# Kernel optimization log

Measured on AMD Instinct MI355X. Metric: run time of the kernel, lower is better.

Reference implementation:

```python
import jax, jax.numpy as jnp
import numpy as np

N, C_TOTAL, C, H, W = 8, 448, 100, 56, 56


def setup_inputs() -> dict:
    key = jax.random.key(0)
    k1, k2, k3, k4 = jax.random.split(key, 4)
    fmaps = jax.random.normal(k1, (N, C_TOTAL, H, W), dtype=jnp.float32)
    select_index = jax.random.randint(k2, (C,), 0, C_TOTAL)
    mean = jax.random.normal(k3, (C, H, W), dtype=jnp.float32)
    # Per-pixel inverse covariance must be PSD so the quadratic form is >= 0
    A = jax.random.normal(k4, (C, C, H, W), dtype=jnp.float32)
    cov = jnp.einsum('cehw,dehw->cdhw', A, A) / jnp.float32(C)  # (C,C,H,W), PSD per pixel
    return {
        'fmaps': fmaps,
        'select_index': select_index,
        'mean': mean,
        'cov': cov,
        'min_score': jnp.float32(0.0),
        'max_score': jnp.float32(50.0),
    }


def reference(fmaps, select_index, mean, cov, min_score, max_score):
    # x_ = fmaps[:, select_index, ...] - mean  -> (N, C, H, W)
    x = fmaps[:, select_index, :, :] - mean[None]
    # left = sum_c x[n,c,h,w] * cov[c,d,h,w]  (per-pixel matvec), avoids (N,C,C,H,W) intermediate
    left = jnp.einsum('nchw,cdhw->ndhw', x, cov)
    # per-pixel Mahalanobis distance
    s_map = jnp.sqrt(jnp.sum(x * left, axis=1))  # (N, H, W)
    # bilinear upsample x4 (torch Upsample align_corners=False == half-pixel linear resize)
    score_map = jax.image.resize(s_map, (s_map.shape[0], 4 * H, 4 * W), method='linear')
    scores = (score_map - min_score) / (max_score - min_score)
    return jnp.squeeze(scores)
```

## Files before the change

### kernel.cpp

```cpp
#include <hip/hip_runtime.h>
#include <math.h>

#define NN 8
#define C_TOTAL 448
#define CC 100
#define HH 56
#define WW 56
#define HW (HH*WW)
#define OH 224
#define OW 224
#define CT 10
#define DT 4
#define NCHUNK (CC/CT)
#define NTILE (HW/64)

__global__ __launch_bounds__(512) void qform_kernel(
    const float* __restrict__ fmaps, const int* __restrict__ sel,
    const float* __restrict__ mean, const float* __restrict__ cov,
    float* __restrict__ qpart)
{
    const int tile  = blockIdx.x % NTILE;
    const int chunk = blockIdx.x / NTILE;
    const int n     = threadIdx.x >> 6;
    const int pix   = tile * 64 + (threadIdx.x & 63);
    const int c0    = chunk * CT;

    __shared__ int s_sel[CC];
    if (threadIdx.x < CC) s_sel[threadIdx.x] = sel[threadIdx.x];
    __syncthreads();

    const float* fm_n = fmaps + (size_t)n * C_TOTAL * HW;

    float xc[CT];
#pragma unroll
    for (int i = 0; i < CT; ++i) {
        const int c = c0 + i;
        xc[i] = fm_n[(size_t)s_sel[c] * HW + pix] - mean[(size_t)c * HW + pix];
    }

    float acc = 0.0f;
    for (int d0 = 0; d0 < CC; d0 += DT) {
        float xd[DT];
#pragma unroll
        for (int j = 0; j < DT; ++j) {
            const int d = d0 + j;
            xd[j] = fm_n[(size_t)s_sel[d] * HW + pix] - mean[(size_t)d * HW + pix];
        }
#pragma unroll
        for (int i = 0; i < CT; ++i) {
            const float* cp = cov + ((size_t)(c0 + i) * CC + d0) * HW + pix;
#pragma unroll
            for (int j = 0; j < DT; ++j) {
                acc = fmaf(xc[i] * xd[j], cp[(size_t)j * HW], acc);
            }
        }
    }
    qpart[((size_t)chunk * NN + n) * HW + pix] = acc;
}

__global__ __launch_bounds__(256) void reduce_kernel(
    const float* __restrict__ qpart, float* __restrict__ smap)
{
    const int idx = blockIdx.x * 256 + threadIdx.x;
    if (idx >= NN * HW) return;
    float s = 0.0f;
#pragma unroll
    for (int k = 0; k < NCHUNK; ++k)
        s += qpart[(size_t)k * NN * HW + idx];
    smap[idx] = sqrtf(fmaxf(s, 0.0f));
}

__global__ __launch_bounds__(256) void upsample_kernel(
    const float* __restrict__ smap,
    const float* __restrict__ minp, const float* __restrict__ maxp,
    float* __restrict__ out)
{
    const int idx = blockIdx.x * 256 + threadIdx.x;
    const int total = NN * OH * OW;
    if (idx >= total) return;

    const int ox = idx % OW;
    const int oy = (idx / OW) % OH;
    const int n  = idx / (OW * OH);

    const float fy = oy * 0.25f - 0.375f;
    const float fx = ox * 0.25f - 0.375f;

    int y0 = (int)floorf(fy);
    int x0 = (int)floorf(fx);
    const float wy = fy - (float)y0;
    const float wx = fx - (float)x0;
    int y1 = min(y0 + 1, HH - 1); y0 = max(y0, 0);
    int x1 = min(x0 + 1, WW - 1); x0 = max(x0, 0);

    const float* s = smap + (size_t)n * HW;
    const float v00 = s[y0 * WW + x0];
    const float v01 = s[y0 * WW + x1];
    const float v10 = s[y1 * WW + x0];
    const float v11 = s[y1 * WW + x1];

    const float v = (1.0f - wy) * ((1.0f - wx) * v00 + wx * v01)
                  +          wy * ((1.0f - wx) * v10 + wx * v11);

    const float mn = *minp;
    const float mx = *maxp;
    out[idx] = (v - mn) / (mx - mn);
}

extern "C" void kernel_launch(void* const* d_in, const int* in_sizes, int n_in,
                              void* d_out, int out_size, void* d_ws, size_t ws_size,
                              hipStream_t stream)
{
    const float* fmaps = (const float*)d_in[0];
    const int*   sel   = (const int*)  d_in[1];
    const float* mean  = (const float*)d_in[2];
    const float* cov   = (const float*)d_in[3];
    const float* minp  = (const float*)d_in[4];
    const float* maxp  = (const float*)d_in[5];
    float* out = (float*)d_out;

    float* qpart = (float*)d_ws;
    float* smap  = qpart + (size_t)NCHUNK * NN * HW;

    qform_kernel<<<NTILE * NCHUNK, 512, 0, stream>>>(fmaps, sel, mean, cov, qpart);
    reduce_kernel<<<(NN * HW + 255) / 256, 256, 0, stream>>>(qpart, smap);

    const int total = NN * OH * OW;
    upsample_kernel<<<(total + 255) / 256, 256, 0, stream>>>(smap, minp, maxp, out);
}
```

Before: 250.9 us.

## Exploit covariance symmetry with balanced row pairs and float4 vectorized streaming

Since each per-pixel covariance is symmetric, the quadratic form reads only the upper triangle, with diagonal terms halved and the sum doubled. Each block handles a balanced pair of rows, r and 99-r, so every thread does the same number of steps. Loads and stores use float4, four pixels per thread. A separate prep kernel gathers and mean-subtracts x once so it is not recomputed in the inner loop. The aim is to roughly halve the dominant cov memory traffic, at the cost of an extra kernel and an x buffer in workspace, and correctness now depends on cov being symmetric.

```diff
diff --git a/kernel.cpp b/kernel.cpp
--- a/kernel.cpp
+++ b/kernel.cpp
@@ -7,67 +7,123 @@
 #define HH 56
 #define WW 56
 #define HW (HH*WW)
+#define NPIX4 (HW/4)
 #define OH 224
 #define OW 224
-#define CT 10
-#define DT 4
-#define NCHUNK (CC/CT)
-#define NTILE (HW/64)
+#define NPAIR 50
+#define NT4 13
+
+__device__ __forceinline__ void fma4(float4& acc, const float4 a, const float4 b) {
+    acc.x = fmaf(a.x, b.x, acc.x);
+    acc.y = fmaf(a.y, b.y, acc.y);
+    acc.z = fmaf(a.z, b.z, acc.z);
+    acc.w = fmaf(a.w, b.w, acc.w);
+}
+
+__global__ __launch_bounds__(256) void prep_x_kernel(
+    const float* __restrict__ fmaps, const int* __restrict__ sel,
+    const float* __restrict__ mean, float* __restrict__ xbuf)
+{
+    const int idx = blockIdx.x * 256 + threadIdx.x;
+    const int total = NN * CC * NPIX4;
+    if (idx >= total) return;
+    const int p4 = idx % NPIX4;
+    const int c  = (idx / NPIX4) % CC;
+    const int n  = idx / (NPIX4 * CC);
+
+    const float4* f4 = (const float4*)fmaps;
+    const float4* m4 = (const float4*)mean;
+    float4*       x4 = (float4*)xbuf;
+
+    const float4 f = f4[((size_t)n * C_TOTAL + sel[c]) * NPIX4 + p4];
+    const float4 m = m4[(size_t)c * NPIX4 + p4];
+    float4 r;
+    r.x = f.x - m.x; r.y = f.y - m.y; r.z = f.z - m.z; r.w = f.w - m.w;
+    x4[((size_t)n * CC + c) * NPIX4 + p4] = r;
+}
 
 __global__ __launch_bounds__(512) void qform_kernel(
-    const float* __restrict__ fmaps, const int* __restrict__ sel,
-    const float* __restrict__ mean, const float* __restrict__ cov,
+    const float* __restrict__ xbuf, const float* __restrict__ cov,
     float* __restrict__ qpart)
 {
-    const int tile  = blockIdx.x % NTILE;
-    const int chunk = blockIdx.x / NTILE;
-    const int n     = threadIdx.x >> 6;
-    const int pix   = tile * 64 + (threadIdx.x & 63);
-    const int c0    = chunk * CT;
+    const int tile = blockIdx.x % NT4;
+    const int r    = blockIdx.x / NT4;
+    const int s    = 99 - r;
+    const int n    = threadIdx.x >> 6;
+    const int p4   = tile * 64 + (threadIdx.x & 63);
+    if (p4 >= NPIX4) return;
 
-    __shared__ int s_sel[CC];
-    if (threadIdx.x < CC) s_sel[threadIdx.x] = sel[threadIdx.x];
-    __syncthreads();
+    const float4* x4  = (const float4*)xbuf + (size_t)n * CC * NPIX4;
+    const float4* c4  = (const float4*)cov;
 
-    const float* fm_n = fmaps + (size_t)n * C_TOTAL * HW;
+    const float4* covr = c4 + ((size_t)r * CC + r) * NPIX4 + p4;
+    const float4* covs = c4 + ((size_t)s * CC + s) * NPIX4 + p4;
+    const float4* xp   = x4 + (size_t)r * NPIX4 + p4;
 
-    float xc[CT];
-#pragma unroll
-    for (int i = 0; i < CT; ++i) {
-        const int c = c0 + i;
-        xc[i] = fm_n[(size_t)s_sel[c] * HW + pix] - mean[(size_t)c * HW + pix];
+    float4 ir = make_float4(0.f, 0.f, 0.f, 0.f);
+    float4 is = make_float4(0.f, 0.f, 0.f, 0.f);
+
+    float4 xr = *xp;
+    {
+        float4 h; h.x = 0.5f*xr.x; h.y = 0.5f*xr.y; h.z = 0.5f*xr.z; h.w = 0.5f*xr.w;
+        fma4(ir, h, *covr);
+    }
+    xp += NPIX4; covr += NPIX4;
+
+#pragma unroll 4
+    for (int d = r + 1; d < s; ++d) {
+        const float4 xd = *xp;
+        fma4(ir, xd, *covr);
+        xp += NPIX4; covr += NPIX4;
     }
 
-    float acc = 0.0f;
-    for (int d0 = 0; d0 < CC; d0 += DT) {
-        float xd[DT];
-#pragma unroll
-        for (int j = 0; j < DT; ++j) {
-            const int d = d0 + j;
-            xd[j] = fm_n[(size_t)s_sel[d] * HW + pix] - mean[(size_t)d * HW + pix];
-        }
-#pragma unroll
-        for (int i = 0; i < CT; ++i) {
-            const float* cp = cov + ((size_t)(c0 + i) * CC + d0) * HW + pix;
-#pragma unroll
-            for (int j = 0; j < DT; ++j) {
-                acc = fmaf(xc[i] * xd[j], cp[(size_t)j * HW], acc);
-            }
-        }
+    float4 xs = *xp;
+    fma4(ir, xs, *covr);
+    {
+        float4 h; h.x = 0.5f*xs.x; h.y = 0.5f*xs.y; h.z = 0.5f*xs.z; h.w = 0.5f*xs.w;
+        fma4(is, h, *covs);
     }
-    qpart[((size_t)chunk * NN + n) * HW + pix] = acc;
+    xp += NPIX4; covr += NPIX4; covs += NPIX4;
+
+#pragma unroll 4
+    for (int d = s + 1; d < CC; ++d) {
+        const float4 xd = *xp;
+        fma4(ir, xd, *covr);
+        fma4(is, xd, *covs);
+        xp += NPIX4; covr += NPIX4; covs += NPIX4;
+    }
+
+    float4 q;
+    q.x = 2.0f * (fmaf(xr.x, ir.x, xs.x * is.x));
+    q.y = 2.0f * (fmaf(xr.y, ir.y, xs.y * is.y));
+    q.z = 2.0f * (fmaf(xr.z, ir.z, xs.z * is.z));
+    q.w = 2.0f * (fmaf(xr.w, ir.w, xs.w * is.w));
+
+    float4* qp = (float4*)qpart;
+    qp[((size_t)r * NN + n) * NPIX4 + p4] = q;
 }
 
 __global__ __launch_bounds__(256) void reduce_kernel(
     const float* __restrict__ qpart, float* __restrict__ smap)
 {
     const int idx = blockIdx.x * 256 + threadIdx.x;
-    if (idx >= NN * HW) return;
-    float s = 0.0f;
+    if (idx >= NN * NPIX4) return;
+    const int p4 = idx % NPIX4;
+    const int n  = idx / NPIX4;
+
+    const float4* qp = (const float4*)qpart;
+    float4 acc = make_float4(0.f, 0.f, 0.f, 0.f);
 #pragma unroll
-    for (int k = 0; k < NCHUNK; ++k)
-        s += qpart[(size_t)k * NN * HW + idx];
-    smap[idx] = sqrtf(fmaxf(s, 0.0f));
+    for (int k = 0; k < NPAIR; ++k) {
+        const float4 v = qp[((size_t)k * NN + n) * NPIX4 + p4];
+        acc.x += v.x; acc.y += v.y; acc.z += v.z; acc.w += v.w;
+    }
+    float4 o;
+    o.x = sqrtf(fmaxf(acc.x, 0.f));
+    o.y = sqrtf(fmaxf(acc.y, 0.f));
+    o.z = sqrtf(fmaxf(acc.z, 0.f));
+    o.w = sqrtf(fmaxf(acc.w, 0.f));
+    ((float4*)smap)[(size_t)n * NPIX4 + p4] = o;
 }
 
 __global__ __launch_bounds__(256) void upsample_kernel(
@@ -119,12 +175,21 @@
     const float* maxp  = (const float*)d_in[5];
     float* out = (float*)d_out;
 
-    float* qpart = (float*)d_ws;
-    float* smap  = qpart + (size_t)NCHUNK * NN * HW;
+    float* xbuf  = (float*)d_ws;
+    float* qpart = xbuf + (size_t)NN * CC * HW;
+    float* smap  = qpart + (size_t)NPAIR * NN * HW;
 
-    qform_kernel<<<NTILE * NCHUNK, 512, 0, stream>>>(fmaps, sel, mean, cov, qpart);
-    reduce_kernel<<<(NN * HW + 255) / 256, 256, 0, stream>>>(qpart, smap);
-
-    const int total = NN * OH * OW;
-    upsample_kernel<<<(total + 255) / 256, 256, 0, stream>>>(smap, minp, maxp, out);
+    {
+        const int total = NN * CC * NPIX4;
+        prep_x_kernel<<<(total + 255) / 256, 256, 0, stream>>>(fmaps, sel, mean, xbuf);
+    }
+    qform_kernel<<<NT4 * NPAIR, 512, 0, stream>>>(xbuf, cov, qpart);
+    {
+        const int total = NN * NPIX4;
+        reduce_kernel<<<(total + 255) / 256, 256, 0, stream>>>(qpart, smap);
+    }
+    {
+        const int total = NN * OH * OW;
+        upsample_kernel<<<(total + 255) / 256, 256, 0, stream>>>(smap, minp, maxp, out);
+    }
 }
```

Result: no change. 247.5 us (-1.4%).
